# Optimization experiments

Measured on AMD Instinct MI355X. Metric: run time of the kernel, lower is better.

Reference implementation:

```python
import jax, jax.numpy as jnp
import numpy as np

B, L, N, HS, HD, C = 4, 200, 160, 768, 256, 16  # batch, bert len, word len, bert hidden, dense hidden, classes


def setup_inputs() -> dict:
    key = jax.random.key(0)
    ks = jax.random.split(key, 8)
    transformer_out = jax.random.normal(ks[0], (B, L + 1, HS), dtype=jnp.float32)
    word_mapback = jnp.sort(jax.random.randint(ks[1], (B, L), 0, N), axis=-1)
    token_length = jnp.maximum(jax.random.randint(ks[2], (B,), 0, N), N // 2)
    length = jnp.maximum(jax.random.randint(ks[3], (B,), 0, L), 3 * L // 4)
    Wd = jax.random.normal(ks[4], (HS, HD), dtype=jnp.float32) * 0.02
    bd = jnp.zeros((HD,), dtype=jnp.float32)
    Wc = jax.random.normal(ks[5], (3 * HD, C), dtype=jnp.float32) * 0.02
    bc = jnp.zeros((C,), dtype=jnp.float32)
    return dict(transformer_out=transformer_out, Wd=Wd, bd=bd, Wc=Wc, bc=bc,
                word_mapback=word_mapback, token_length=token_length, length=length)


def reference(transformer_out, Wd, bd, Wc, bc, word_mapback, token_length, length):
    # mask over bert positions (after dropping CLS at index 0)
    bert_indi = (jnp.arange(L) < length[:, None]).astype(jnp.float32)[..., None]   # [B,L,1]
    h = transformer_out[:, 1:L + 1, :] * bert_indi                                  # [B,L,HS]
    onehot = jax.nn.one_hot(word_mapback, N, dtype=jnp.float32) * bert_indi         # [B,L,N]
    dense_h = h @ Wd + bd                                                           # [B,L,HD]
    # word-piece -> word mean pooling (one-hot bmm + count normalize)
    pooled = jnp.einsum('bln,blh->bnh', onehot, dense_h)                             # [B,N,HD]
    wnt = onehot.sum(axis=1)                                                         # [B,N]
    pooled = pooled / jnp.where(wnt == 0, 1.0, wnt)[..., None]
    # candidate (i,j) upper-triangular valid-span mask
    tok_mask = (jnp.arange(N) < token_length[:, None]).astype(jnp.float32)           # [B,N]
    cand = jnp.triu(jnp.ones((N, N), jnp.float32))[None] * (tok_mask[:, None, :] * tok_mask[:, :, None])  # [B,N,N]
    # boundary features: [start_repr ; end_repr]
    boundary = jnp.concatenate([
        jnp.broadcast_to(pooled[:, :, None, :], (B, N, N, HD)),
        jnp.broadcast_to(pooled[:, None, :, :], (B, N, N, HD))], axis=-1) * cand[..., None]
    # span sums: span[b,i,k,d] = sum_{i<=j<=k} pooled[b,j,d]*tok_mask[b,j], via prefix sums
    pv = jnp.cumsum(pooled * tok_mask[..., None], axis=1)                            # P[k]
    pv0 = jnp.concatenate([jnp.zeros((B, 1, HD), pv.dtype), pv[:, :-1]], axis=1)     # P[i-1]
    span = (pv[:, None, :, :] - pv0[:, :, None, :]) * cand[..., None]                # [B,N,N,HD]
    # span averaging: divide by span length (k - i + 1), clamped to 1 elsewhere
    diff = jnp.arange(1, N + 1)[None, :] - jnp.arange(N)[:, None]                    # diff[i,k] = k+1-i
    span = span / jnp.where(diff > 0, diff, 1).astype(jnp.float32)[None, :, :, None]
    table = jnp.concatenate([boundary, span], axis=-1)                               # [B,N,N,3*HD]
    logits = (table @ Wc + bc) * cand[..., None]                                     # [B,N,N,C]
    return logits
```

## Files before the change

kernel.cpp:

```cpp
#include <hip/hip_runtime.h>

#define B 4
#define L 200
#define N 160
#define HS 768
#define HD 256
#define C 16

#define KP 784
#define WJ 48
#define NROW (B * N)
#define WCT_STRIDE 260
#define KH 80

__global__ __launch_bounds__(256) void prep_kernel(
    const float* __restrict__ TO,
    const float* __restrict__ Wd,
    const float* __restrict__ bd,
    const float* __restrict__ Wc,
    const int*   __restrict__ wm,
    const int*   __restrict__ lengths,
    float* __restrict__ hs_s,
    float* __restrict__ Wfull)
{
    const int blk = blockIdx.x;
    const int t = threadIdx.x;

    if (blk < NROW) {
        const int row = blk;
        const int b = row / N, n = row % N;
        const int len = lengths[b];

        __shared__ int smap[L];
        for (int e = t; e < L; e += 256) smap[e] = wm[b * L + e];
        __syncthreads();

        int lo = 0, hi = L;
        while (lo < hi) { int m = (lo + hi) >> 1; if (smap[m] < n) lo = m + 1; else hi = m; }
        int lo2 = lo, hi2 = L;
        while (lo2 < hi2) { int m = (lo2 + hi2) >> 1; if (smap[m] < n + 1) lo2 = m + 1; else hi2 = m; }
        const int start = lo < len ? lo : len;
        const int stop  = lo2 < len ? lo2 : len;
        const int cnt   = stop - start;
        const float ci  = (cnt > 0) ? 1.0f / (float)cnt : 0.0f;

        float a0 = 0.f, a1 = 0.f, a2 = 0.f;
        const float* base = TO + ((size_t)b * (L + 1) + 1) * HS;
        for (int l = start; l < stop; ++l) {
            const float* r = base + (size_t)l * HS;
            a0 += r[t]; a1 += r[t + 256]; a2 += r[t + 512];
        }
        float* hr = hs_s + (size_t)row * KP;
        hr[t] = a0 * ci; hr[t + 256] = a1 * ci; hr[t + 512] = a2 * ci;
        if (t < 16) hr[768 + t] = (t == 0 && cnt > 0) ? 1.0f : 0.0f;
    } else if (blk < NROW + 144) {
        const int wb = blk - NROW;
        const int kb = wb / 3;
        const int m  = wb % 3;

        __shared__ float wcT[16 * WCT_STRIDE];
        for (int e = t; e < HD * C; e += 256) {
            const int d = e >> 4, c = e & 15;
            wcT[c * WCT_STRIDE + d] = Wc[(size_t)(m * HD + d) * C + c];
        }
        __syncthreads();

        const int kl = t >> 4, c = t & 15;
        const int k = kb * 16 + kl;
        const float4* wd4 = (const float4*)(Wd + (size_t)k * HD);
        const float4* wc4 = (const float4*)(wcT + c * WCT_STRIDE);
        float acc = 0.f;
        #pragma unroll 8
        for (int q = 0; q < HD / 4; ++q) {
            const float4 a = wd4[q];
            const float4 w = wc4[q];
            acc += a.x * w.x + a.y * w.y + a.z * w.z + a.w * w.w;
        }
        Wfull[(size_t)k * WJ + m * 16 + c] = acc;
    } else {
        if (t < WJ) {
            const int m = t >> 4, c = t & 15;
            const float4* bd4 = (const float4*)bd;
            float acc = 0.f;
            #pragma unroll 8
            for (int q = 0; q < HD / 4; ++q) {
                const float4 w = bd4[q];
                const int d = 4 * q;
                acc += w.x * Wc[(size_t)(m * HD + d) * C + c]
                     + w.y * Wc[(size_t)(m * HD + d + 1) * C + c]
                     + w.z * Wc[(size_t)(m * HD + d + 2) * C + c]
                     + w.w * Wc[(size_t)(m * HD + d + 3) * C + c];
            }
            Wfull[(size_t)768 * WJ + t] = acc;
        }
        for (int e = t; e < WJ * 15; e += 256) {
            const int k = 769 + e / WJ, j = e % WJ;
            Wfull[(size_t)k * WJ + j] = 0.f;
        }
    }
}

__global__ __launch_bounds__(192) void gemm_kernel(
    const float* __restrict__ hs_s,
    const float* __restrict__ Wfull,
    const int*   __restrict__ token_length,
    float* __restrict__ AB,
    float* __restrict__ T)
{
    const int t  = threadIdx.x;
    const int tj = t % WJ;
    const int tr = t / WJ;
    const int row = blockIdx.x * 4 + tr;

    const float4* in = (const float4*)(hs_s + (size_t)row * KP);
    const float*  wf = Wfull + tj;
    float acc = 0.f;
    #pragma unroll 7
    for (int q = 0; q < KP / 4; ++q) {
        const float4 v = in[q];
        acc += v.x * wf[(size_t)(4 * q) * WJ]     + v.y * wf[(size_t)(4 * q + 1) * WJ]
             + v.z * wf[(size_t)(4 * q + 2) * WJ] + v.w * wf[(size_t)(4 * q + 3) * WJ];
    }
    const int b = row / N, n = row % N;
    if (tj < 32) {
        AB[(size_t)row * 32 + tj] = acc;
    } else {
        T[(size_t)row * 16 + (tj - 32)] = (n < token_length[b]) ? acc : 0.f;
    }
}

__global__ __launch_bounds__(256) void finalize_kernel(
    const float* __restrict__ AB,
    const float* __restrict__ T,
    const float* __restrict__ bc,
    const int*   __restrict__ token_length,
    float4* __restrict__ out)
{
    const int it = blockIdx.x;
    const int kh = blockIdx.y;
    const int b  = blockIdx.z;
    const int t  = threadIdx.x;
    const int tl = token_length[b];

    __shared__ float sT[N * 16];
    __shared__ float sB[KH * 16];
    __shared__ float sA[8 * 16];
    __shared__ float sS[(N + 1) * 16];
    __shared__ float pref[16 * 16];

    {
        const float4* T4 = (const float4*)(T + (size_t)b * N * 16);
        float4* sT4 = (float4*)sT;
        for (int e = t; e < N * 4; e += 256) sT4[e] = T4[e];
    }
    for (int e = t; e < KH * 4; e += 256) {
        const int kl = e >> 2, cq = e & 3;
        *(float4*)&sB[kl * 16 + cq * 4] =
            *(const float4*)&AB[((size_t)b * N + kh * KH + kl) * 32 + 16 + cq * 4];
    }
    if (t < 32) {
        const int il = t >> 2, cq = t & 3;
        *(float4*)&sA[il * 16 + cq * 4] =
            *(const float4*)&AB[((size_t)b * N + it * 8 + il) * 32 + cq * 4];
    }
    if (t < 16) sS[t] = 0.f;
    __syncthreads();

    const int c = t & 15, g = t >> 4;
    const int nb = g * 10;
    {
        float run = 0.f;
        for (int u = 0; u < 10; ++u) {
            run += sT[(nb + u) * 16 + c];
            sS[(nb + u + 1) * 16 + c] = run;
        }
        pref[g * 16 + c] = run;
    }
    __syncthreads();
    if (t < 16) {
        float off = 0.f;
        for (int g2 = 0; g2 < 16; ++g2) {
            const float tmp = pref[g2 * 16 + t];
            pref[g2 * 16 + t] = off;
            off += tmp;
        }
    }
    __syncthreads();
    {
        const float off = pref[g * 16 + c];
        for (int u = 0; u < 10; ++u) sS[(nb + u + 1) * 16 + c] += off;
    }
    __syncthreads();

    for (int q = 0; q < 10; ++q) {
        const int qid = t + q * 256;
        const int cq  = qid & 3;
        const int kl  = (qid >> 2) % KH;
        const int il  = (qid >> 2) / KH;
        const int i   = it * 8 + il;
        const int k   = kh * KH + kl;

        float4 v = {0.f, 0.f, 0.f, 0.f};
        if ((i <= k) & (i < tl) & (k < tl)) {
            const float4 a   = *(const float4*)&sA[il * 16 + cq * 4];
            const float4 bb  = *(const float4*)&sB[kl * 16 + cq * 4];
            const float4 sk  = *(const float4*)&sS[(k + 1) * 16 + cq * 4];
            const float4 si  = *(const float4*)&sS[i * 16 + cq * 4];
            const float4 bcq = *(const float4*)&bc[cq * 4];
            const float inv = 1.0f / (float)(k - i + 1);
            v.x = a.x + bb.x + (sk.x - si.x) * inv + bcq.x;
            v.y = a.y + bb.y + (sk.y - si.y) * inv + bcq.y;
            v.z = a.z + bb.z + (sk.z - si.z) * inv + bcq.z;
            v.w = a.w + bb.w + (sk.w - si.w) * inv + bcq.w;
        }
        out[((size_t)(b * N + i) * N + k) * 4 + cq] = v;
    }
}

extern "C" void kernel_launch(void* const* d_in, const int* in_sizes, int n_in,
                              void* d_out, int out_size, void* d_ws, size_t ws_size,
                              hipStream_t stream) {
    const float* TO    = (const float*)d_in[0];
    const float* Wd    = (const float*)d_in[1];
    const float* bd    = (const float*)d_in[2];
    const float* Wc    = (const float*)d_in[3];
    const float* bc    = (const float*)d_in[4];
    const int*   wm    = (const int*)d_in[5];
    const int*   tokl  = (const int*)d_in[6];
    const int*   lenp  = (const int*)d_in[7];

    float* ws    = (float*)d_ws;
    float* hs_s  = ws;
    float* Wfull = hs_s + (size_t)NROW * KP;
    float* AB    = Wfull + (size_t)KP * WJ;
    float* T     = AB + (size_t)NROW * 32;

    prep_kernel<<<NROW + 144 + 1, 256, 0, stream>>>(TO, Wd, bd, Wc, wm, lenp, hs_s, Wfull);
    gemm_kernel<<<NROW / 4, 192, 0, stream>>>(hs_s, Wfull, tokl, AB, T);
    finalize_kernel<<<dim3(20, 2, B), 256, 0, stream>>>(AB, T, bc, tokl, (float4*)d_out);
}
```

Measured before the change: 35.65 us.

## Fuse three kernels into one persistent kernel with software grid barriers

Replaces the prep, gemm and finalize launches with one 160-block kernel that synchronises stages through flag-based grid barriers in global memory. Each block pools its four rows into LDS and runs the row GEMM straight from LDS with a split-K reduction, so the pooled hidden states are never written to global memory. This removes two launch gaps and the hs_s round trip. In exchange the work runs on only 160 blocks and relies on all of them being co-resident, and the barrier spin loops are bounded by a guard counter.

```diff
diff --git a/kernel.cpp b/kernel.cpp
--- a/kernel.cpp
+++ b/kernel.cpp
@@ -10,61 +10,106 @@
 #define KP 784
 #define WJ 48
 #define NROW (B * N)
+#define NBLK 160
+#define KSL4 196
 #define WCT_STRIDE 260
 #define KH 80
 
-__global__ __launch_bounds__(256) void prep_kernel(
+__device__ __forceinline__ void grid_bar(unsigned* flags, int blk, int t, unsigned phase) {
+    __syncthreads();
+    if (t == 0) {
+        __builtin_amdgcn_fence(__ATOMIC_RELEASE, "agent");
+        __hip_atomic_store(&flags[blk], phase, __ATOMIC_RELAXED, __HIP_MEMORY_SCOPE_AGENT);
+    }
+    if (t < NBLK) {
+        int guard = 0;
+        while (__hip_atomic_load(&flags[t], __ATOMIC_RELAXED, __HIP_MEMORY_SCOPE_AGENT) < phase
+               && guard < (1 << 22)) {
+            __builtin_amdgcn_s_sleep(4);
+            ++guard;
+        }
+    }
+    __builtin_amdgcn_fence(__ATOMIC_ACQUIRE, "agent");
+    __syncthreads();
+}
+
+__global__ __launch_bounds__(256) void mega_kernel(
     const float* __restrict__ TO,
     const float* __restrict__ Wd,
     const float* __restrict__ bd,
     const float* __restrict__ Wc,
+    const float* __restrict__ bc,
     const int*   __restrict__ wm,
-    const int*   __restrict__ lengths,
-    float* __restrict__ hs_s,
-    float* __restrict__ Wfull)
+    const int*   __restrict__ tokl,
+    const int*   __restrict__ lenp,
+    unsigned* __restrict__ flags,
+    float* __restrict__ Wfull,
+    float* __restrict__ AB,
+    float* __restrict__ Tg,
+    float4* __restrict__ out)
 {
     const int blk = blockIdx.x;
-    const int t = threadIdx.x;
-
-    if (blk < NROW) {
-        const int row = blk;
-        const int b = row / N, n = row % N;
-        const int len = lengths[b];
-
-        __shared__ int smap[L];
-        for (int e = t; e < L; e += 256) smap[e] = wm[b * L + e];
-        __syncthreads();
-
+    const int t   = threadIdx.x;
+
+    __shared__ float uni[7296];
+    __shared__ int   smap[L];
+    __shared__ int   sstart[4], sstop[4];
+    __shared__ float sci[4];
+
+    if (t == 0)
+        __hip_atomic_store(&flags[blk], 0u, __ATOMIC_RELAXED, __HIP_MEMORY_SCOPE_AGENT);
+    if (t < NBLK) {
+        int guard = 0;
+        while (__hip_atomic_load(&flags[t], __ATOMIC_RELAXED, __HIP_MEMORY_SCOPE_AGENT) > 1u
+               && guard < (1 << 22)) {
+            __builtin_amdgcn_s_sleep(4);
+            ++guard;
+        }
+    }
+    __syncthreads();
+
+    const int row0 = blk * 4;
+    const int b    = row0 / N;
+    const int len  = lenp[b];
+    for (int e = t; e < L; e += 256) smap[e] = wm[b * L + e];
+    __syncthreads();
+    if (t < 4) {
+        const int n = (row0 % N) + t;
         int lo = 0, hi = L;
         while (lo < hi) { int m = (lo + hi) >> 1; if (smap[m] < n) lo = m + 1; else hi = m; }
         int lo2 = lo, hi2 = L;
         while (lo2 < hi2) { int m = (lo2 + hi2) >> 1; if (smap[m] < n + 1) lo2 = m + 1; else hi2 = m; }
         const int start = lo < len ? lo : len;
         const int stop  = lo2 < len ? lo2 : len;
-        const int cnt   = stop - start;
-        const float ci  = (cnt > 0) ? 1.0f / (float)cnt : 0.0f;
-
+        sstart[t] = start; sstop[t] = stop;
+        sci[t] = (stop > start) ? 1.0f / (float)(stop - start) : 0.0f;
+    }
+    __syncthreads();
+
+    float* hsL = uni;
+    for (int r = 0; r < 4; ++r) {
+        const int start = sstart[r], stop = sstop[r];
+        const float ci = sci[r];
         float a0 = 0.f, a1 = 0.f, a2 = 0.f;
         const float* base = TO + ((size_t)b * (L + 1) + 1) * HS;
         for (int l = start; l < stop; ++l) {
-            const float* r = base + (size_t)l * HS;
-            a0 += r[t]; a1 += r[t + 256]; a2 += r[t + 512];
-        }
-        float* hr = hs_s + (size_t)row * KP;
-        hr[t] = a0 * ci; hr[t + 256] = a1 * ci; hr[t + 512] = a2 * ci;
-        if (t < 16) hr[768 + t] = (t == 0 && cnt > 0) ? 1.0f : 0.0f;
-    } else if (blk < NROW + 144) {
-        const int wb = blk - NROW;
-        const int kb = wb / 3;
-        const int m  = wb % 3;
-
-        __shared__ float wcT[16 * WCT_STRIDE];
+            const float* rr = base + (size_t)l * HS;
+            a0 += rr[t]; a1 += rr[t + 256]; a2 += rr[t + 512];
+        }
+        hsL[r * KP + t]       = a0 * ci;
+        hsL[r * KP + t + 256] = a1 * ci;
+        hsL[r * KP + t + 512] = a2 * ci;
+        if (t < 16) hsL[r * KP + 768 + t] = (t == 0 && stop > start) ? 1.0f : 0.0f;
+    }
+
+    if (blk < 144) {
+        float* wcT = uni + 3136;
+        const int kb = blk / 3, m = blk % 3;
         for (int e = t; e < HD * C; e += 256) {
             const int d = e >> 4, c = e & 15;
             wcT[c * WCT_STRIDE + d] = Wc[(size_t)(m * HD + d) * C + c];
         }
         __syncthreads();
-
         const int kl = t >> 4, c = t & 15;
         const int k = kb * 16 + kl;
         const float4* wd4 = (const float4*)(Wd + (size_t)k * HD);
@@ -77,15 +122,14 @@
             acc += a.x * w.x + a.y * w.y + a.z * w.z + a.w * w.w;
         }
         Wfull[(size_t)k * WJ + m * 16 + c] = acc;
-    } else {
+    } else if (blk == 144) {
         if (t < WJ) {
             const int m = t >> 4, c = t & 15;
-            const float4* bd4 = (const float4*)bd;
             float acc = 0.f;
             #pragma unroll 8
             for (int q = 0; q < HD / 4; ++q) {
-                const float4 w = bd4[q];
                 const int d = 4 * q;
+                const float4 w = *(const float4*)(bd + d);
                 acc += w.x * Wc[(size_t)(m * HD + d) * C + c]
                      + w.y * Wc[(size_t)(m * HD + d + 1) * C + c]
                      + w.z * Wc[(size_t)(m * HD + d + 2) * C + c]
@@ -98,70 +142,61 @@
             Wfull[(size_t)k * WJ + j] = 0.f;
         }
     }
-}
-
-__global__ __launch_bounds__(192) void gemm_kernel(
-    const float* __restrict__ hs_s,
-    const float* __restrict__ Wfull,
-    const int*   __restrict__ token_length,
-    float* __restrict__ AB,
-    float* __restrict__ T)
-{
-    const int t  = threadIdx.x;
-    const int tj = t % WJ;
-    const int tr = t / WJ;
-    const int row = blockIdx.x * 4 + tr;
-
-    const float4* in = (const float4*)(hs_s + (size_t)row * KP);
-    const float*  wf = Wfull + tj;
-    float acc = 0.f;
-    #pragma unroll 7
-    for (int q = 0; q < KP / 4; ++q) {
-        const float4 v = in[q];
-        acc += v.x * wf[(size_t)(4 * q) * WJ]     + v.y * wf[(size_t)(4 * q + 1) * WJ]
-             + v.z * wf[(size_t)(4 * q + 2) * WJ] + v.w * wf[(size_t)(4 * q + 3) * WJ];
-    }
-    const int b = row / N, n = row % N;
-    if (tj < 32) {
-        AB[(size_t)row * 32 + tj] = acc;
-    } else {
-        T[(size_t)row * 16 + (tj - 32)] = (n < token_length[b]) ? acc : 0.f;
-    }
-}
-
-__global__ __launch_bounds__(256) void finalize_kernel(
-    const float* __restrict__ AB,
-    const float* __restrict__ T,
-    const float* __restrict__ bc,
-    const int*   __restrict__ token_length,
-    float4* __restrict__ out)
-{
-    const int it = blockIdx.x;
-    const int kh = blockIdx.y;
-    const int b  = blockIdx.z;
-    const int t  = threadIdx.x;
-    const int tl = token_length[b];
-
-    __shared__ float sT[N * 16];
-    __shared__ float sB[KH * 16];
-    __shared__ float sA[8 * 16];
-    __shared__ float sS[(N + 1) * 16];
-    __shared__ float pref[16 * 16];
+
+    grid_bar(flags, blk, t, 1u);
+
+    float* pLDS = uni + 3136;
+    if (t < 192) {
+        const int jq = t % 12, r = (t / 12) % 4, ks = t / 48;
+        const float* wf = Wfull + jq * 4;
+        float4 acc = {0.f, 0.f, 0.f, 0.f};
+        const int kbeg = ks * KSL4;
+        #pragma unroll 4
+        for (int kk = 0; kk < KSL4; ++kk) {
+            const int k = kbeg + kk;
+            const float  h = hsL[r * KP + k];
+            const float4 w = *(const float4*)(wf + (size_t)k * WJ);
+            acc.x += h * w.x; acc.y += h * w.y; acc.z += h * w.z; acc.w += h * w.w;
+        }
+        *(float4*)&pLDS[(ks * 4 + r) * WJ + jq * 4] = acc;
+    }
+    __syncthreads();
+    if (t < 192) {
+        const int r = t / WJ, j = t % WJ;
+        const float v = pLDS[r * WJ + j] + pLDS[(4 + r) * WJ + j]
+                      + pLDS[(8 + r) * WJ + j] + pLDS[(12 + r) * WJ + j];
+        const int row = row0 + r;
+        const int n = row % N;
+        if (j < 32) AB[(size_t)row * 32 + j] = v;
+        else        Tg[(size_t)row * 16 + (j - 32)] = (n < tokl[b]) ? v : 0.f;
+    }
+
+    grid_bar(flags, blk, t, 2u);
+
+    const int it = blk % 20;
+    const int kh = (blk / 20) % 2;
+    const int b2 = blk / 40;
+    const int tl = tokl[b2];
+    float* sT   = uni;
+    float* sB   = uni + 2560;
+    float* sA   = uni + 3840;
+    float* sS   = uni + 3968;
+    float* pref = uni + 6544;
 
     {
-        const float4* T4 = (const float4*)(T + (size_t)b * N * 16);
+        const float4* T4 = (const float4*)(Tg + (size_t)b2 * N * 16);
         float4* sT4 = (float4*)sT;
         for (int e = t; e < N * 4; e += 256) sT4[e] = T4[e];
     }
     for (int e = t; e < KH * 4; e += 256) {
         const int kl = e >> 2, cq = e & 3;
         *(float4*)&sB[kl * 16 + cq * 4] =
-            *(const float4*)&AB[((size_t)b * N + kh * KH + kl) * 32 + 16 + cq * 4];
+            *(const float4*)&AB[((size_t)b2 * N + kh * KH + kl) * 32 + 16 + cq * 4];
     }
     if (t < 32) {
         const int il = t >> 2, cq = t & 3;
         *(float4*)&sA[il * 16 + cq * 4] =
-            *(const float4*)&AB[((size_t)b * N + it * 8 + il) * 32 + cq * 4];
+            *(const float4*)&AB[((size_t)b2 * N + it * 8 + il) * 32 + cq * 4];
     }
     if (t < 16) sS[t] = 0.f;
     __syncthreads();
@@ -213,29 +248,28 @@
             v.z = a.z + bb.z + (sk.z - si.z) * inv + bcq.z;
             v.w = a.w + bb.w + (sk.w - si.w) * inv + bcq.w;
         }
-        out[((size_t)(b * N + i) * N + k) * 4 + cq] = v;
+        out[((size_t)(b2 * N + i) * N + k) * 4 + cq] = v;
     }
 }
 
 extern "C" void kernel_launch(void* const* d_in, const int* in_sizes, int n_in,
                               void* d_out, int out_size, void* d_ws, size_t ws_size,
                               hipStream_t stream) {
-    const float* TO    = (const float*)d_in[0];
-    const float* Wd    = (const float*)d_in[1];
-    const float* bd    = (const float*)d_in[2];
-    const float* Wc    = (const float*)d_in[3];
-    const float* bc    = (const float*)d_in[4];
-    const int*   wm    = (const int*)d_in[5];
-    const int*   tokl  = (const int*)d_in[6];
-    const int*   lenp  = (const int*)d_in[7];
-
-    float* ws    = (float*)d_ws;
-    float* hs_s  = ws;
-    float* Wfull = hs_s + (size_t)NROW * KP;
+    const float* TO   = (const float*)d_in[0];
+    const float* Wd   = (const float*)d_in[1];
+    const float* bd   = (const float*)d_in[2];
+    const float* Wc   = (const float*)d_in[3];
+    const float* bc   = (const float*)d_in[4];
+    const int*   wm   = (const int*)d_in[5];
+    const int*   tokl = (const int*)d_in[6];
+    const int*   lenp = (const int*)d_in[7];
+
+    unsigned* flags = (unsigned*)d_ws;
+    float* base  = (float*)d_ws + 256;
+    float* Wfull = base;
     float* AB    = Wfull + (size_t)KP * WJ;
-    float* T     = AB + (size_t)NROW * 32;
-
-    prep_kernel<<<NROW + 144 + 1, 256, 0, stream>>>(TO, Wd, bd, Wc, wm, lenp, hs_s, Wfull);
-    gemm_kernel<<<NROW / 4, 192, 0, stream>>>(hs_s, Wfull, tokl, AB, T);
-    finalize_kernel<<<dim3(20, 2, B), 256, 0, stream>>>(AB, T, bc, tokl, (float4*)d_out);
+    float* Tg    = AB + (size_t)NROW * 32;
+
+    mega_kernel<<<NBLK, 256, 0, stream>>>(TO, Wd, bd, Wc, bc, wm, tokl, lenp,
+                                          flags, Wfull, AB, Tg, (float4*)d_out);
 }
```

Result: slower. 52.78 us (+48.1%).

## Fuse word pooling into projection GEMM, keeping pooled rows in shared memory

Applied to the files above, without the earlier changes.

Pooling of word-piece rows moves out of the prep kernel and into the GEMM kernel. Each block now pools one word row into LDS and projects it against Wfull right away, using a 4-way K split and an LDS reduction. This removes the global round trip of the pooled hs_s buffer (640x784 floats) and changes how work is split across the kernels. In exchange, Wfull must finish before pooling can start, pooling no longer overlaps with Wfull construction, and the binary search runs on a single thread.

```diff
diff --git a/kernel.cpp b/kernel.cpp
--- a/kernel.cpp
+++ b/kernel.cpp
@@ -13,50 +13,18 @@
 #define WCT_STRIDE 260
 #define KH 80
 
-__global__ __launch_bounds__(256) void prep_kernel(
-    const float* __restrict__ TO,
+__global__ __launch_bounds__(256) void wfull_kernel(
     const float* __restrict__ Wd,
     const float* __restrict__ bd,
     const float* __restrict__ Wc,
-    const int*   __restrict__ wm,
-    const int*   __restrict__ lengths,
-    float* __restrict__ hs_s,
     float* __restrict__ Wfull)
 {
     const int blk = blockIdx.x;
     const int t = threadIdx.x;
 
-    if (blk < NROW) {
-        const int row = blk;
-        const int b = row / N, n = row % N;
-        const int len = lengths[b];
-
-        __shared__ int smap[L];
-        for (int e = t; e < L; e += 256) smap[e] = wm[b * L + e];
-        __syncthreads();
-
-        int lo = 0, hi = L;
-        while (lo < hi) { int m = (lo + hi) >> 1; if (smap[m] < n) lo = m + 1; else hi = m; }
-        int lo2 = lo, hi2 = L;
-        while (lo2 < hi2) { int m = (lo2 + hi2) >> 1; if (smap[m] < n + 1) lo2 = m + 1; else hi2 = m; }
-        const int start = lo < len ? lo : len;
-        const int stop  = lo2 < len ? lo2 : len;
-        const int cnt   = stop - start;
-        const float ci  = (cnt > 0) ? 1.0f / (float)cnt : 0.0f;
-
-        float a0 = 0.f, a1 = 0.f, a2 = 0.f;
-        const float* base = TO + ((size_t)b * (L + 1) + 1) * HS;
-        for (int l = start; l < stop; ++l) {
-            const float* r = base + (size_t)l * HS;
-            a0 += r[t]; a1 += r[t + 256]; a2 += r[t + 512];
-        }
-        float* hr = hs_s + (size_t)row * KP;
-        hr[t] = a0 * ci; hr[t + 256] = a1 * ci; hr[t + 512] = a2 * ci;
-        if (t < 16) hr[768 + t] = (t == 0 && cnt > 0) ? 1.0f : 0.0f;
-    } else if (blk < NROW + 144) {
-        const int wb = blk - NROW;
-        const int kb = wb / 3;
-        const int m  = wb % 3;
+    if (blk < 144) {
+        const int kb = blk / 3;
+        const int m  = blk % 3;
 
         __shared__ float wcT[16 * WCT_STRIDE];
         for (int e = t; e < HD * C; e += 256) {
@@ -80,12 +48,11 @@
     } else {
         if (t < WJ) {
             const int m = t >> 4, c = t & 15;
-            const float4* bd4 = (const float4*)bd;
             float acc = 0.f;
             #pragma unroll 8
             for (int q = 0; q < HD / 4; ++q) {
-                const float4 w = bd4[q];
                 const int d = 4 * q;
+                const float4 w = *(const float4*)(bd + d);
                 acc += w.x * Wc[(size_t)(m * HD + d) * C + c]
                      + w.y * Wc[(size_t)(m * HD + d + 1) * C + c]
                      + w.z * Wc[(size_t)(m * HD + d + 2) * C + c]
@@ -100,32 +67,78 @@
     }
 }
 
-__global__ __launch_bounds__(192) void gemm_kernel(
-    const float* __restrict__ hs_s,
+__global__ __launch_bounds__(256) void poolgemm_kernel(
+    const float* __restrict__ TO,
     const float* __restrict__ Wfull,
+    const int*   __restrict__ wm,
+    const int*   __restrict__ lengths,
     const int*   __restrict__ token_length,
     float* __restrict__ AB,
-    float* __restrict__ T)
+    float* __restrict__ Tg)
 {
-    const int t  = threadIdx.x;
-    const int tj = t % WJ;
-    const int tr = t / WJ;
-    const int row = blockIdx.x * 4 + tr;
-
-    const float4* in = (const float4*)(hs_s + (size_t)row * KP);
-    const float*  wf = Wfull + tj;
-    float acc = 0.f;
-    #pragma unroll 7
-    for (int q = 0; q < KP / 4; ++q) {
-        const float4 v = in[q];
-        acc += v.x * wf[(size_t)(4 * q) * WJ]     + v.y * wf[(size_t)(4 * q + 1) * WJ]
-             + v.z * wf[(size_t)(4 * q + 2) * WJ] + v.w * wf[(size_t)(4 * q + 3) * WJ];
-    }
-    const int b = row / N, n = row % N;
-    if (tj < 32) {
-        AB[(size_t)row * 32 + tj] = acc;
-    } else {
-        T[(size_t)row * 16 + (tj - 32)] = (n < token_length[b]) ? acc : 0.f;
+    const int row = blockIdx.x;
+    const int t   = threadIdx.x;
+    const int b   = row / N, n = row % N;
+
+    __shared__ int   smap[L];
+    __shared__ int   s_start, s_stop;
+    __shared__ float s_ci;
+    __shared__ float hsL[KP];
+    __shared__ float pLDS[4 * WJ];
+
+    for (int e = t; e < L; e += 256) smap[e] = wm[b * L + e];
+    __syncthreads();
+
+    if (t == 0) {
+        const int len = lengths[b];
+        int lo = 0, hi = L;
+        while (lo < hi) { int m = (lo + hi) >> 1; if (smap[m] < n) lo = m + 1; else hi = m; }
+        int lo2 = lo, hi2 = L;
+        while (lo2 < hi2) { int m = (lo2 + hi2) >> 1; if (smap[m] < n + 1) lo2 = m + 1; else hi2 = m; }
+        const int start = lo < len ? lo : len;
+        const int stop  = lo2 < len ? lo2 : len;
+        s_start = start; s_stop = stop;
+        s_ci = (stop > start) ? 1.0f / (float)(stop - start) : 0.0f;
+    }
+    __syncthreads();
+
+    {
+        const int start = s_start, stop = s_stop;
+        const float ci = s_ci;
+        float a0 = 0.f, a1 = 0.f, a2 = 0.f;
+        const float* base = TO + ((size_t)b * (L + 1) + 1) * HS;
+        for (int l = start; l < stop; ++l) {
+            const float* r = base + (size_t)l * HS;
+            a0 += r[t]; a1 += r[t + 256]; a2 += r[t + 512];
+        }
+        hsL[t]       = a0 * ci;
+        hsL[t + 256] = a1 * ci;
+        hsL[t + 512] = a2 * ci;
+        if (t < 16) hsL[768 + t] = (t == 0 && stop > start) ? 1.0f : 0.0f;
+    }
+    __syncthreads();
+
+    if (t < 192) {
+        const int j  = t % WJ;
+        const int ks = t / WJ;
+        const int k0 = ks * 196;
+        const float* wf = Wfull + j;
+        float acc = 0.f;
+        #pragma unroll 7
+        for (int q = 0; q < 49; ++q) {
+            const int k = k0 + 4 * q;
+            const float4 h = *(const float4*)&hsL[k];
+            acc += h.x * wf[(size_t)k * WJ]       + h.y * wf[(size_t)(k + 1) * WJ]
+                 + h.z * wf[(size_t)(k + 2) * WJ] + h.w * wf[(size_t)(k + 3) * WJ];
+        }
+        pLDS[ks * WJ + j] = acc;
+    }
+    __syncthreads();
+
+    if (t < WJ) {
+        const float v = pLDS[t] + pLDS[WJ + t] + pLDS[2 * WJ + t] + pLDS[3 * WJ + t];
+        if (t < 32) AB[(size_t)row * 32 + t] = v;
+        else        Tg[(size_t)row * 16 + (t - 32)] = (n < token_length[b]) ? v : 0.f;
     }
 }
 
@@ -230,12 +243,11 @@
     const int*   lenp  = (const int*)d_in[7];
 
     float* ws    = (float*)d_ws;
-    float* hs_s  = ws;
-    float* Wfull = hs_s + (size_t)NROW * KP;
+    float* Wfull = ws;
     float* AB    = Wfull + (size_t)KP * WJ;
-    float* T     = AB + (size_t)NROW * 32;
-
-    prep_kernel<<<NROW + 144 + 1, 256, 0, stream>>>(TO, Wd, bd, Wc, wm, lenp, hs_s, Wfull);
-    gemm_kernel<<<NROW / 4, 192, 0, stream>>>(hs_s, Wfull, tokl, AB, T);
-    finalize_kernel<<<dim3(20, 2, B), 256, 0, stream>>>(AB, T, bc, tokl, (float4*)d_out);
-}
+    float* Tg    = AB + (size_t)NROW * 32;
+
+    wfull_kernel<<<145, 256, 0, stream>>>(Wd, bd, Wc, Wfull);
+    poolgemm_kernel<<<NROW, 256, 0, stream>>>(TO, Wfull, wm, lenp, tokl, AB, Tg);
+    finalize_kernel<<<dim3(20, 2, B), 256, 0, stream>>>(AB, Tg, bc, tokl, (float4*)d_out);
+}
```

Result: faster. 30.26 us (-15.1%).
